# Kernel optimization log

Hardware: AMD Instinct MI355X
Metric: run time of the kernel (lower is better)

The kernel has to match this reference:

```python
import jax, jax.numpy as jnp
import numpy as np

B, N, IN_F, OUT_F, H = 4, 2048, 256, 256, 8
NH = OUT_F // H  # 32
SLOPE = 0.2
NEG_INF = -9e15


def setup_inputs() -> dict:
    key = jax.random.key(0)
    k1, k2, k3, k4 = jax.random.split(key, 4)
    h = jax.random.normal(k1, (B, N, IN_F), jnp.float32)
    adj = jax.random.randint(k2, (B, N, N), 0, 2).astype(jnp.int32)
    # xavier_uniform with gain 1.414
    gw = 1.414 * np.sqrt(6.0 / (IN_F + H * NH))
    W = jax.random.uniform(k3, (IN_F, H * NH), jnp.float32, -gw, gw)
    ga = 1.414 * np.sqrt(6.0 / (2 * NH + 1))
    a = jax.random.uniform(k4, (2 * NH, 1), jnp.float32, -ga, ga)
    return {"h": h, "adj": adj, "W": W, "a": a}


def reference(h, adj, W, a):
    Wh = h @ W                              # [B, N, H*NH]
    # Faithful to torch .view: raw memory reinterpretation, not a transpose.
    Wh = Wh.reshape(B, H, N, NH)            # [B, H, N, NH]
    Wh1 = Wh @ a[:NH]                       # [B, H, N, 1]
    Wh2 = Wh @ a[NH:]                       # [B, H, N, 1]
    e = Wh1 + jnp.swapaxes(Wh2, 2, 3)       # [B, H, N, N] additive scores
    e = jnp.where(e >= 0, e, SLOPE * e)     # leaky relu
    e = jnp.where(adj[:, None] > 0, e, NEG_INF)
    attn = jax.nn.softmax(e, axis=-1)       # [B, H, N, N]
    h_prime = attn @ Wh                     # [B, H, N, NH]
    h_prime = h_prime.reshape(B, N, OUT_F)  # raw reshape, matches torch .view
    return jax.nn.elu(h_prime)
```

## Files before the change

kernel.cpp:

```cpp
#include <hip/hip_runtime.h>
#include <hip/hip_bf16.h>

#define B_    4
#define N_    2048
#define INF_  256
#define OUTF_ 256
#define H_    8
#define NH_   32
#define BH_   (B_ * H_)
#define ROWS_ (B_ * N_)
#define VSZ_  (N_ * NH_)

typedef float  f32x4 __attribute__((ext_vector_type(4)));
typedef short  s16x8 __attribute__((ext_vector_type(8)));

static __device__ __forceinline__ short f2bf(float x) {
    union { __hip_bfloat16 b; unsigned short u; } cv;
    cv.b = __float2bfloat16(x);
    return (short)cv.u;
}

__global__ __launch_bounds__(256) void prep(const int* __restrict__ adj,
                                            unsigned int* __restrict__ adjw,
                                            const float* __restrict__ h,
                                            const float* __restrict__ W,
                                            short* __restrict__ hb,
                                            short* __restrict__ Wf) {
    const int blk = blockIdx.x;
    const int tid = threadIdx.x;
    if (blk < 2048) {
        const int idx = blk * 256 + tid;
        const int4* p = (const int4*)(adj + (size_t)idx * 32);
        unsigned int w = 0;
#pragma unroll
        for (int q = 0; q < 8; ++q) {
            int4 v = p[q];
            w |= (v.x != 0 ? 1u : 0u) << (q * 4 + 0);
            w |= (v.y != 0 ? 1u : 0u) << (q * 4 + 1);
            w |= (v.z != 0 ? 1u : 0u) << (q * 4 + 2);
            w |= (v.w != 0 ? 1u : 0u) << (q * 4 + 3);
        }
        adjw[idx] = w;
    } else if (blk < 3072) {
        const int t = (blk - 2048) * 256 + tid;
        const float4* src = (const float4*)(h + (size_t)t * 8);
        float4 v0 = src[0], v1 = src[1];
        float vv[8] = {v0.x, v0.y, v0.z, v0.w, v1.x, v1.y, v1.z, v1.w};
        s16x8 o;
#pragma unroll
        for (int i = 0; i < 8; ++i) o[i] = f2bf(vv[i]);
        *(s16x8*)(hb + (size_t)t * 8) = o;
    } else {
        const int u = (blk - 3072) * 256 + tid;
        const int lane = u & 63, nf = (u >> 6) & 15, kt = u >> 10;
        const float* src = W + (size_t)(kt * 32 + (lane >> 4) * 8) * 256 +
                           nf * 16 + (lane & 15);
        s16x8 o;
#pragma unroll
        for (int i = 0; i < 8; ++i) o[i] = f2bf(src[(size_t)i * 256]);
        *(s16x8*)(Wf + (size_t)u * 8) = o;
    }
}

__global__ __launch_bounds__(256) void gemm_st(const short* __restrict__ hb,
                                               const short* __restrict__ Wf,
                                               const float* __restrict__ a,
                                               float* __restrict__ Wh,
                                               float2* __restrict__ sE,
                                               float2* __restrict__ tE) {
    const int bm  = blockIdx.x * 64;
    const int bn4 = blockIdx.y * 4;
    const int tid = threadIdx.x;
    const int wv = tid >> 6, l = tid & 63;
    const int lr = l & 15, lg = l >> 4;
    const int arow = bm + wv * 16 + lr;

    f32x4 acc[4] = {};
    const s16x8* wf = (const s16x8*)Wf;
    const s16x8* ha = (const s16x8*)(hb + (size_t)arow * 256 + lg * 8);

#pragma unroll
    for (int kt = 0; kt < 8; ++kt) {
        s16x8 av = ha[kt * 4];
#pragma unroll
        for (int nf = 0; nf < 4; ++nf) {
            s16x8 b = wf[(size_t)(kt * 16 + bn4 + nf) * 64 + l];
            acc[nf] = __builtin_amdgcn_mfma_f32_16x16x32_bf16(av, b, acc[nf], 0, 0, 0);
        }
    }
#pragma unroll
    for (int nf = 0; nf < 4; ++nf)
#pragma unroll
        for (int r = 0; r < 4; ++r)
            Wh[(size_t)(bm + wv * 16 + 4 * lg + r) * 256 +
               (size_t)(bn4 + nf) * 16 + lr] = acc[nf][r];

    const float a1lo = a[lr],      a1hi = a[16 + lr];
    const float a2lo = a[32 + lr], a2hi = a[48 + lr];
#pragma unroll
    for (int k = 0; k < 2; ++k) {
#pragma unroll
        for (int r = 0; r < 4; ++r) {
            float ps = acc[2 * k][r] * a1lo + acc[2 * k + 1][r] * a1hi;
            float pt = acc[2 * k][r] * a2lo + acc[2 * k + 1][r] * a2hi;
#pragma unroll
            for (int d = 1; d < 16; d <<= 1) {
                ps += __shfl_xor(ps, d);
                pt += __shfl_xor(pt, d);
            }
            if (lr == 0) {
                const int R  = bm + wv * 16 + 4 * lg + r;
                const int b  = R >> 11, rin = R & 2047;
                const int hh = rin >> 8, rr = rin & 255;
                const int n  = rr * 8 + (bn4 >> 1) + k;
                const int g  = ((b * 8 + hh) << 11) + n;
                sE[g] = make_float2(__expf(ps), __expf(0.2f * ps));
                tE[g] = make_float2(__expf(pt), __expf(0.2f * pt));
            }
        }
    }
}

__global__ __launch_bounds__(256) void vconv(const float* __restrict__ Wh,
                                             short* __restrict__ Vb) {
    const int t = blockIdx.x * 256 + threadIdx.x;
    const int lane = t & 63;
    const int nt   = (t >> 6) & 1;
    const int jt   = (t >> 7) & 63;
    const int bh   = t >> 13;
    const float* src = Wh + (size_t)bh * VSZ_ +
                       (size_t)(jt * 32 + (lane >> 4) * 8) * NH_ +
                       nt * 16 + (lane & 15);
    s16x8 v;
#pragma unroll
    for (int i = 0; i < 8; ++i) v[i] = f2bf(src[(size_t)i * NH_]);
    *(s16x8*)(Vb + (size_t)t * 8) = v;
}

__global__ __launch_bounds__(256) void attn_kernel(const short* __restrict__ Vb,
                                                   const float2* __restrict__ sE,
                                                   const float2* __restrict__ tE,
                                                   const unsigned int* __restrict__ adjw,
                                                   float* __restrict__ out) {
    const int bh = blockIdx.y;
    const int b  = bh >> 3;
    const int i0 = blockIdx.x * 64;
    const int tid = threadIdx.x;
    const int wv = tid >> 6;
    const int l  = tid & 63;
    const int lr = l & 15;
    const int lg = l >> 4;

    __shared__ int    adjL[64][68];
    __shared__ float4 ts4[1024];

    {
        const int4* ab = (const int4*)(adjw + (size_t)(b * N_ + i0) * 64);
#pragma unroll
        for (int k = 0; k < 4; ++k) {
            int idx4 = tid + k * 256;
            int4 v = ab[idx4];
            *(int4*)&adjL[idx4 >> 4][(idx4 << 2) & 63] = v;
        }
    }
    {
        const float4* tsrc = (const float4*)(tE + (size_t)bh * N_);
#pragma unroll
        for (int k = 0; k < 4; ++k) ts4[tid + k * 256] = tsrc[tid + k * 256];
    }
    const float2 es = sE[(size_t)bh * N_ + i0 + wv * 16 + lr];
    __syncthreads();

    s16x8 bOnes;
#pragma unroll
    for (int i = 0; i < 8; ++i) bOnes[i] = (lr == 0) ? (short)0x3F80 : (short)0;

    const s16x8* vb = (const s16x8*)(Vb + (size_t)bh * 65536);

    s16x8 nb0 = vb[l];
    s16x8 nb1 = vb[64 + l];
    f32x4 acc0 = {0.f, 0.f, 0.f, 0.f};
    f32x4 acc1 = {0.f, 0.f, 0.f, 0.f};
    f32x4 acc2 = {0.f, 0.f, 0.f, 0.f};

    for (int jt = 0; jt < 64; ++jt) {
        s16x8 b0 = nb0, b1 = nb1;
        if (jt < 63) {
            nb0 = vb[(jt + 1) * 128 + l];
            nb1 = vb[(jt + 1) * 128 + 64 + l];
        }
        const unsigned wsh = ((unsigned)adjL[wv * 16 + lr][jt]) >> (lg * 8);
        const int jb = jt * 16 + lg * 4;
        float4 q0 = ts4[jb + 0];
        float4 q1 = ts4[jb + 1];
        float4 q2 = ts4[jb + 2];
        float4 q3 = ts4[jb + 3];
        float p[8];
        p[0] = fmaxf(es.x * q0.x, es.y * q0.y);
        p[1] = fmaxf(es.x * q0.z, es.y * q0.w);
        p[2] = fmaxf(es.x * q1.x, es.y * q1.y);
        p[3] = fmaxf(es.x * q1.z, es.y * q1.w);
        p[4] = fmaxf(es.x * q2.x, es.y * q2.y);
        p[5] = fmaxf(es.x * q2.z, es.y * q2.w);
        p[6] = fmaxf(es.x * q3.x, es.y * q3.y);
        p[7] = fmaxf(es.x * q3.z, es.y * q3.w);
        unsigned pu[8];
#pragma unroll
        for (int i = 0; i < 8; ++i) {
            const int m = ((int)(wsh << (31 - i))) >> 31;
            pu[i] = __float_as_uint(p[i]) & (unsigned)m;
        }
        union { unsigned u[4]; s16x8 v; } af;
#pragma unroll
        for (int q = 0; q < 4; ++q)
            asm("v_cvt_pk_bf16_f32 %0, %1, %2"
                : "=v"(af.u[q])
                : "v"(__uint_as_float(pu[2 * q])), "v"(__uint_as_float(pu[2 * q + 1])));

        acc0 = __builtin_amdgcn_mfma_f32_16x16x32_bf16(af.v, b0, acc0, 0, 0, 0);
        acc1 = __builtin_amdgcn_mfma_f32_16x16x32_bf16(af.v, b1, acc1, 0, 0, 0);
        acc2 = __builtin_amdgcn_mfma_f32_16x16x32_bf16(af.v, bOnes, acc2, 0, 0, 0);
    }

    float* obase = out + (size_t)bh * VSZ_;
#pragma unroll
    for (int r = 0; r < 4; ++r) {
        const int rloc = 4 * lg + r;
        const float rsum = __shfl(acc2[r], (l & 48));
        const float ir = 1.0f / rsum;
        const int row = i0 + wv * 16 + rloc;
        float v0 = acc0[r] * ir;
        float v1 = acc1[r] * ir;
        v0 = v0 > 0.f ? v0 : expm1f(v0);
        v1 = v1 > 0.f ? v1 : expm1f(v1);
        obase[(size_t)row * NH_ + lr]      = v0;
        obase[(size_t)row * NH_ + 16 + lr] = v1;
    }
}

extern "C" void kernel_launch(void* const* d_in, const int* in_sizes, int n_in,
                              void* d_out, int out_size, void* d_ws, size_t ws_size,
                              hipStream_t stream) {
    const float* h   = (const float*)d_in[0];
    const int*   adj = (const int*)d_in[1];
    const float* W   = (const float*)d_in[2];
    const float* a   = (const float*)d_in[3];
    float* out = (float*)d_out;

    char* ws = (char*)d_ws;
    float*  Wh = (float*)ws;
    char*   p1 = ws + (size_t)ROWS_ * OUTF_ * 4;
    float2* sE = (float2*)p1;
    float2* tE = (float2*)(p1 + (size_t)BH_ * N_ * 8);
    unsigned int* adjw = (unsigned int*)(p1 + 2 * (size_t)BH_ * N_ * 8);
    short* Vb = (short*)(p1 + 2 * (size_t)BH_ * N_ * 8 + (size_t)B_ * N_ * 64 * 4);
    short* hb = (short*)((char*)Vb + (size_t)BH_ * VSZ_ * 2);
    short* Wf = (short*)((char*)hb + (size_t)ROWS_ * INF_ * 2);

    prep<<<3104, 256, 0, stream>>>(adj, adjw, h, W, hb, Wf);
    gemm_st<<<dim3(ROWS_ / 64, OUTF_ / 64), 256, 0, stream>>>(hb, Wf, a, Wh, sE, tE);
    vconv<<<(BH_ * N_ * NH_ / 8) / 256, 256, 0, stream>>>(Wh, Vb);
    attn_kernel<<<dim3(N_ / 64, BH_), 256, 0, stream>>>(Vb, sE, tE, adjw, out);
}
```

Measured before the change: 156.5 us.

## Fuse V bf16 conversion into GEMM epilogue and unroll attention loop by two

```diff
diff --git a/kernel.cpp b/kernel.cpp
--- a/kernel.cpp
+++ b/kernel.cpp
@@ -12,6 +12,7 @@
 #define VSZ_  (N_ * NH_)
 
 typedef float  f32x4 __attribute__((ext_vector_type(4)));
+typedef float  f32x2 __attribute__((ext_vector_type(2)));
 typedef short  s16x8 __attribute__((ext_vector_type(8)));
 
 static __device__ __forceinline__ short f2bf(float x) {
@@ -62,12 +63,12 @@
     }
 }
 
-__global__ __launch_bounds__(256) void gemm_st(const short* __restrict__ hb,
-                                               const short* __restrict__ Wf,
-                                               const float* __restrict__ a,
-                                               float* __restrict__ Wh,
-                                               float2* __restrict__ sE,
-                                               float2* __restrict__ tE) {
+__global__ __launch_bounds__(256) void gemm_stv(const short* __restrict__ hb,
+                                                const short* __restrict__ Wf,
+                                                const float* __restrict__ a,
+                                                float2* __restrict__ sE,
+                                                float2* __restrict__ tE,
+                                                short* __restrict__ Vb) {
     const int bm  = blockIdx.x * 64;
     const int bn4 = blockIdx.y * 4;
     const int tid = threadIdx.x;
@@ -88,12 +89,23 @@
             acc[nf] = __builtin_amdgcn_mfma_f32_16x16x32_bf16(av, b, acc[nf], 0, 0, 0);
         }
     }
-#pragma unroll
-    for (int nf = 0; nf < 4; ++nf)
-#pragma unroll
-        for (int r = 0; r < 4; ++r)
-            Wh[(size_t)(bm + wv * 16 + 4 * lg + r) * 256 +
-               (size_t)(bn4 + nf) * 16 + lr] = acc[nf][r];
+
+    {
+        const int bh  = bm >> 8;
+        const int rr0 = (bm & 255) + wv * 16 + 4 * lg;
+        short* vout = Vb + (size_t)bh * 65536;
+#pragma unroll
+        for (int nf = 0; nf < 4; ++nf) {
+            const int nt = nf & 1;
+            const int ch = (bn4 + nf) >> 1;
+#pragma unroll
+            for (int r = 0; r < 4; ++r) {
+                const int rr = rr0 + r;
+                vout[((rr >> 2) * 2 + nt) * 512 + ((rr & 3) * 16 + lr) * 8 + ch] =
+                    f2bf(acc[nf][r]);
+            }
+        }
+    }
 
     const float a1lo = a[lr],      a1hi = a[16 + lr];
     const float a2lo = a[32 + lr], a2hi = a[48 + lr];
@@ -121,22 +133,6 @@
     }
 }
 
-__global__ __launch_bounds__(256) void vconv(const float* __restrict__ Wh,
-                                             short* __restrict__ Vb) {
-    const int t = blockIdx.x * 256 + threadIdx.x;
-    const int lane = t & 63;
-    const int nt   = (t >> 6) & 1;
-    const int jt   = (t >> 7) & 63;
-    const int bh   = t >> 13;
-    const float* src = Wh + (size_t)bh * VSZ_ +
-                       (size_t)(jt * 32 + (lane >> 4) * 8) * NH_ +
-                       nt * 16 + (lane & 15);
-    s16x8 v;
-#pragma unroll
-    for (int i = 0; i < 8; ++i) v[i] = f2bf(src[(size_t)i * NH_]);
-    *(s16x8*)(Vb + (size_t)t * 8) = v;
-}
-
 __global__ __launch_bounds__(256) void attn_kernel(const short* __restrict__ Vb,
                                                    const float2* __restrict__ sE,
                                                    const float2* __restrict__ tE,
@@ -168,7 +164,8 @@
 #pragma unroll
         for (int k = 0; k < 4; ++k) ts4[tid + k * 256] = tsrc[tid + k * 256];
     }
-    const float2 es = sE[(size_t)bh * N_ + i0 + wv * 16 + lr];
+    const float2 esl = sE[(size_t)bh * N_ + i0 + wv * 16 + lr];
+    const f32x2 es2 = {esl.x, esl.y};
     __syncthreads();
 
     s16x8 bOnes;
@@ -177,38 +174,32 @@
 
     const s16x8* vb = (const s16x8*)(Vb + (size_t)bh * 65536);
 
-    s16x8 nb0 = vb[l];
-    s16x8 nb1 = vb[64 + l];
     f32x4 acc0 = {0.f, 0.f, 0.f, 0.f};
     f32x4 acc1 = {0.f, 0.f, 0.f, 0.f};
     f32x4 acc2 = {0.f, 0.f, 0.f, 0.f};
 
-    for (int jt = 0; jt < 64; ++jt) {
-        s16x8 b0 = nb0, b1 = nb1;
-        if (jt < 63) {
-            nb0 = vb[(jt + 1) * 128 + l];
-            nb1 = vb[(jt + 1) * 128 + 64 + l];
-        }
-        const unsigned wsh = ((unsigned)adjL[wv * 16 + lr][jt]) >> (lg * 8);
-        const int jb = jt * 16 + lg * 4;
+    auto tile = [&](int jtc, s16x8 B0, s16x8 B1) {
+        const unsigned wsh = ((unsigned)adjL[wv * 16 + lr][jtc]) >> (lg * 8);
+        const int jb = jtc * 16 + lg * 4;
         float4 q0 = ts4[jb + 0];
         float4 q1 = ts4[jb + 1];
         float4 q2 = ts4[jb + 2];
         float4 q3 = ts4[jb + 3];
-        float p[8];
-        p[0] = fmaxf(es.x * q0.x, es.y * q0.y);
-        p[1] = fmaxf(es.x * q0.z, es.y * q0.w);
-        p[2] = fmaxf(es.x * q1.x, es.y * q1.y);
-        p[3] = fmaxf(es.x * q1.z, es.y * q1.w);
-        p[4] = fmaxf(es.x * q2.x, es.y * q2.y);
-        p[5] = fmaxf(es.x * q2.z, es.y * q2.w);
-        p[6] = fmaxf(es.x * q3.x, es.y * q3.y);
-        p[7] = fmaxf(es.x * q3.z, es.y * q3.w);
+        f32x2 pr[8];
+        pr[0] = es2 * (f32x2){q0.x, q0.y};
+        pr[1] = es2 * (f32x2){q0.z, q0.w};
+        pr[2] = es2 * (f32x2){q1.x, q1.y};
+        pr[3] = es2 * (f32x2){q1.z, q1.w};
+        pr[4] = es2 * (f32x2){q2.x, q2.y};
+        pr[5] = es2 * (f32x2){q2.z, q2.w};
+        pr[6] = es2 * (f32x2){q3.x, q3.y};
+        pr[7] = es2 * (f32x2){q3.z, q3.w};
         unsigned pu[8];
 #pragma unroll
         for (int i = 0; i < 8; ++i) {
+            const float p = fmaxf(pr[i].x, pr[i].y);
             const int m = ((int)(wsh << (31 - i))) >> 31;
-            pu[i] = __float_as_uint(p[i]) & (unsigned)m;
+            pu[i] = __float_as_uint(p) & (unsigned)m;
         }
         union { unsigned u[4]; s16x8 v; } af;
 #pragma unroll
@@ -216,10 +207,21 @@
             asm("v_cvt_pk_bf16_f32 %0, %1, %2"
                 : "=v"(af.u[q])
                 : "v"(__uint_as_float(pu[2 * q])), "v"(__uint_as_float(pu[2 * q + 1])));
-
-        acc0 = __builtin_amdgcn_mfma_f32_16x16x32_bf16(af.v, b0, acc0, 0, 0, 0);
-        acc1 = __builtin_amdgcn_mfma_f32_16x16x32_bf16(af.v, b1, acc1, 0, 0, 0);
+        acc0 = __builtin_amdgcn_mfma_f32_16x16x32_bf16(af.v, B0, acc0, 0, 0, 0);
+        acc1 = __builtin_amdgcn_mfma_f32_16x16x32_bf16(af.v, B1, acc1, 0, 0, 0);
         acc2 = __builtin_amdgcn_mfma_f32_16x16x32_bf16(af.v, bOnes, acc2, 0, 0, 0);
+    };
+
+    s16x8 cb0 = vb[l], cb1 = vb[64 + l];
+    for (int jt = 0; jt < 64; jt += 2) {
+        s16x8 nb0 = vb[(jt + 1) * 128 + l];
+        s16x8 nb1 = vb[(jt + 1) * 128 + 64 + l];
+        tile(jt, cb0, cb1);
+        if (jt < 62) {
+            cb0 = vb[(jt + 2) * 128 + l];
+            cb1 = vb[(jt + 2) * 128 + 64 + l];
+        }
+        tile(jt + 1, nb0, nb1);
     }
 
     float* obase = out + (size_t)bh * VSZ_;
@@ -248,17 +250,15 @@
     float* out = (float*)d_out;
 
     char* ws = (char*)d_ws;
-    float*  Wh = (float*)ws;
-    char*   p1 = ws + (size_t)ROWS_ * OUTF_ * 4;
-    float2* sE = (float2*)p1;
-    float2* tE = (float2*)(p1 + (size_t)BH_ * N_ * 8);
-    unsigned int* adjw = (unsigned int*)(p1 + 2 * (size_t)BH_ * N_ * 8);
-    short* Vb = (short*)(p1 + 2 * (size_t)BH_ * N_ * 8 + (size_t)B_ * N_ * 64 * 4);
-    short* hb = (short*)((char*)Vb + (size_t)BH_ * VSZ_ * 2);
-    short* Wf = (short*)((char*)hb + (size_t)ROWS_ * INF_ * 2);
+    float2* sE = (float2*)ws;
+    float2* tE = (float2*)(ws + (size_t)BH_ * N_ * 8);
+    unsigned int* adjw = (unsigned int*)(ws + 2 * (size_t)BH_ * N_ * 8);
+    char* p2 = ws + 2 * (size_t)BH_ * N_ * 8 + (size_t)B_ * N_ * 64 * 4;
+    short* Vb = (short*)p2;
+    short* hb = (short*)(p2 + (size_t)BH_ * VSZ_ * 2);
+    short* Wf = (short*)(p2 + (size_t)BH_ * VSZ_ * 2 + (size_t)ROWS_ * INF_ * 2);
 
     prep<<<3104, 256, 0, stream>>>(adj, adjw, h, W, hb, Wf);
-    gemm_st<<<dim3(ROWS_ / 64, OUTF_ / 64), 256, 0, stream>>>(hb, Wf, a, Wh, sE, tE);
-    vconv<<<(BH_ * N_ * NH_ / 8) / 256, 256, 0, stream>>>(Wh, Vb);
+    gemm_stv<<<dim3(ROWS_ / 64, OUTF_ / 64), 256, 0, stream>>>(hb, Wf, a, sE, tE, Vb);
     attn_kernel<<<dim3(N_ / 64, BH_), 256, 0, stream>>>(Vb, sE, tE, adjw, out);
 }
```

Result: faster. 147.7 us (-5.6%).
